# Kernel tuning notes

Measured on AMD Instinct MI355X. Metric: run time of the kernel, lower is better.

## Reference

```python
import jax, jax.numpy as jnp
import numpy as np

N_HEADS = 16
PROJ_DIM = 64  # per-head dim
DIM = N_HEADS * PROJ_DIM  # 1024


def setup_inputs() -> dict:
    key = jax.random.key(0)
    k1, k2, k3, k4, k5 = jax.random.split(key, 5)
    N, L = 2, 2048
    scale = 1.0 / np.sqrt(DIM)
    return {
        "query": jax.random.normal(k1, (N, L, DIM), dtype=jnp.float32),
        "key": jax.random.normal(k2, (N, L, DIM), dtype=jnp.float32),
        "Wq": jax.random.normal(k3, (DIM, DIM), dtype=jnp.float32) * scale,
        "Wk": jax.random.normal(k4, (DIM, DIM), dtype=jnp.float32) * scale,
        "Wv": jax.random.normal(k5, (DIM, DIM), dtype=jnp.float32) * scale,
    }


def reference(query, key, Wq, Wk, Wv):
    # Causal linear-complexity attention (mask=True branch, left_first=False).
    N, Lq, _ = query.shape
    Lk = key.shape[1]
    H, Dh = N_HEADS, PROJ_DIM
    # torch Linear: x @ W.T ; reshape to (N, H, L, Dh)
    q = (query @ Wq.T).reshape(N, Lq, H, Dh).transpose(0, 2, 1, 3)
    k = (key @ Wk.T).reshape(N, Lk, H, Dh).transpose(0, 2, 1, 3)
    v = (key @ Wv.T).reshape(N, Lk, H, Dh).transpose(0, 2, 1, 3)
    q = jax.nn.softmax(q, axis=-1)
    k = jax.nn.softmax(k, axis=-1)
    # right[t] = sum_{s<=t} k_s^T v_s  : (N,H,Lk,Dh,Dh) cumulative outer products
    S = jnp.cumsum(jnp.einsum('nhti,nhtj->nhtij', k, v), axis=2)
    out = jnp.einsum('nhti,nhtij->nhtj', q, S)  # (N,H,Lq,Dh)
    return out.transpose(0, 2, 1, 3).reshape(N, Lq, H * Dh)
```

## Files before the change

kernel.cpp:

```cpp
#include <hip/hip_runtime.h>


constexpr int DIM  = 1024;
constexpr int H    = 16;
constexpr int DH   = 64;
constexpr int LSEQ = 2048;
constexpr int NB   = 2;
constexpr int MTOK = NB * LSEQ;
constexpr int CS   = 64;
constexpr int NC   = LSEQ / CS;

typedef __bf16 bf16x8 __attribute__((ext_vector_type(8)));
typedef float floatx4 __attribute__((ext_vector_type(4)));
typedef unsigned short ushort_t;

__device__ __forceinline__ ushort_t f2bf(float f) {
  unsigned int u = __float_as_uint(f);
  u += 0x7FFFu + ((u >> 16) & 1u);
  return (ushort_t)(u >> 16);
}

__device__ __forceinline__ void async16(void* lds, const void* g) {
  __builtin_amdgcn_global_load_lds(
      (const __attribute__((address_space(1))) unsigned int*)g,
      (__attribute__((address_space(3))) unsigned int*)lds, 16, 0, 0);
}

__device__ __forceinline__ bf16x8 tfrag(const unsigned int* T, int row, int uoff) {
  union { bf16x8 v; unsigned int u[4]; } r;
  const unsigned int* p = T + row * 33 + uoff;
  r.u[0] = p[0]; r.u[1] = p[1]; r.u[2] = p[2]; r.u[3] = p[3];
  return r.v;
}

__device__ __forceinline__ void transpose_tile(const ushort_t* g, unsigned int* TT, int tid) {
  const int ic = tid & 7, tp = tid >> 3;
  const ushort_t* r0 = g + (size_t)(2 * tp) * DIM + ic * 8;
  union { uint4 q; ushort_t u[8]; } a0, a1;
  a0.q = *(const uint4*)r0;
  a1.q = *(const uint4*)(r0 + DIM);
#pragma unroll
  for (int j = 0; j < 8; j++)
    TT[(8 * ic + j) * 33 + tp] = (unsigned int)a0.u[j] | ((unsigned int)a1.u[j] << 16);
}

__global__ __launch_bounds__(256) void cast_all(const float* __restrict__ q,
                                                const float* __restrict__ k,
                                                const float* __restrict__ wq,
                                                const float* __restrict__ wk,
                                                const float* __restrict__ wv,
                                                ushort_t* __restrict__ xbf,
                                                ushort_t* __restrict__ wbf) {
  const int seg = blockIdx.y;
  const float* src;
  ushort_t* dst;
  int n4;
  if (seg == 0)      { src = q;  dst = xbf;                  n4 = (4 << 20) / 4; }
  else if (seg == 1) { src = k;  dst = xbf + (4 << 20);      n4 = (4 << 20) / 4; }
  else if (seg == 2) { src = wq; dst = wbf;                  n4 = (1 << 20) / 4; }
  else if (seg == 3) { src = wk; dst = wbf + (1 << 20);      n4 = (1 << 20) / 4; }
  else               { src = wv; dst = wbf + (2 << 20);      n4 = (1 << 20) / 4; }
  for (int i = blockIdx.x * 256 + threadIdx.x; i < n4; i += gridDim.x * 256) {
    const float4 f = ((const float4*)src)[i];
    ((ushort4*)dst)[i] = make_ushort4(f2bf(f.x), f2bf(f.y), f2bf(f.z), f2bf(f.w));
  }
}

struct Stage2 { ushort_t As[256 * 32]; ushort_t Ws[256 * 32]; };
union SMemU { Stage2 st[2]; ushort_t CsB[64 * 264]; };

__global__ __launch_bounds__(512, 2) void gemm_fused(const ushort_t* __restrict__ xbf,
                                                     const ushort_t* __restrict__ wbf,
                                                     ushort_t* __restrict__ qp,
                                                     ushort_t* __restrict__ kp,
                                                     ushort_t* __restrict__ vp) {
  __shared__ SMemU sm;
  const int tid = threadIdx.x;

  const int xcd   = blockIdx.x & 7;
  const int local = blockIdx.x >> 3;
  const int T     = xcd * 24 + local;
  const int z     = T >> 6;
  const int rem   = T & 63;
  const int bm    = (rem >> 2) * 256;
  const int bn    = (rem & 3) * 256;

  const ushort_t* A = xbf + (z ? (size_t)(4 << 20) : 0);
  const ushort_t* W = wbf + (size_t)z * (1 << 20);
  ushort_t* C = (z == 0) ? qp : ((z == 1) ? kp : vp);

  const int lane  = tid & 63;
  const int wid   = tid >> 6;
  const int wr    = wid >> 2, wc = wid & 3;
  const int row16 = lane & 15, quad = lane >> 4;

  floatx4 acc[8][4] = {};

  const int srow = tid >> 2;
  const int lc   = (tid & 3) ^ ((srow ^ (srow >> 2)) & 3);
  const ushort_t* pA0 = A + (size_t)(bm + srow) * DIM + lc * 8;
  const ushort_t* pA1 = A + (size_t)(bm + 128 + srow) * DIM + lc * 8;
  const ushort_t* pW0 = W + (size_t)(bn + srow) * DIM + lc * 8;
  const ushort_t* pW1 = W + (size_t)(bn + 128 + srow) * DIM + lc * 8;

#define STAGEB(B, kt)                                         \
  {                                                           \
    ushort_t* As_ = sm.st[B].As;                              \
    ushort_t* Ws_ = sm.st[B].Ws;                              \
    const int ko = (kt) * 32;                                 \
    async16(As_ + tid * 8,         pA0 + ko);                 \
    async16(As_ + (tid + 512) * 8, pA1 + ko);                 \
    async16(Ws_ + tid * 8,         pW0 + ko);                 \
    async16(Ws_ + (tid + 512) * 8, pW1 + ko);                 \
  }

  const int xq    = quad ^ ((row16 ^ (row16 >> 2)) & 3);
  const int aBase = (wr * 128 + row16) * 32 + xq * 8;
  const int bBase = (wc * 64 + row16) * 32 + xq * 8;

  bf16x8 aF0[8], bF0[4], aF1[8], bF1[4];

#define READB(B, AF, BF)                                                      \
  {                                                                           \
    _Pragma("unroll")                                                         \
    for (int mt = 0; mt < 8; mt++)                                            \
      AF[mt] = *(const bf16x8*)&sm.st[B].As[aBase + mt * 512];                \
    _Pragma("unroll")                                                         \
    for (int nt = 0; nt < 4; nt++)                                            \
      BF[nt] = *(const bf16x8*)&sm.st[B].Ws[bBase + nt * 512];                \
  }

#define MFMAB(AF, BF)                                                         \
  {                                                                           \
    _Pragma("unroll")                                                         \
    for (int mt = 0; mt < 8; mt++)                                            \
      _Pragma("unroll")                                                       \
      for (int nt = 0; nt < 4; nt++)                                          \
        acc[mt][nt] = __builtin_amdgcn_mfma_f32_16x16x32_bf16(                \
            AF[mt], BF[nt], acc[mt][nt], 0, 0, 0);                            \
  }

  STAGEB(0, 0);
  STAGEB(1, 1);
  asm volatile("s_waitcnt vmcnt(4)" ::: "memory");
  __builtin_amdgcn_s_barrier();
  READB(0, aF0, bF0);

#pragma unroll
  for (int kt = 0; kt < 32; ++kt) {
    asm volatile("s_waitcnt lgkmcnt(0)" ::: "memory");
    __builtin_amdgcn_s_barrier();
    if (kt + 2 < 32) {
      if ((kt & 1) == 0) { STAGEB(0, kt + 2); } else { STAGEB(1, kt + 2); }
    }
    if (kt + 1 < 32) {
      if (kt + 2 < 32) { asm volatile("s_waitcnt vmcnt(4)" ::: "memory"); }
      else             { asm volatile("s_waitcnt vmcnt(0)" ::: "memory"); }
      __builtin_amdgcn_s_barrier();
      if ((kt & 1) == 0) { READB(1, aF1, bF1); } else { READB(0, aF0, bF0); }
    }
    if ((kt & 1) == 0) { MFMAB(aF0, bF0); } else { MFMAB(aF1, bF1); }
  }
#undef STAGEB
#undef READB
#undef MFMAB

  if (z < 2) {
#pragma unroll
    for (int mt = 0; mt < 8; mt++)
#pragma unroll
      for (int r = 0; r < 4; r++) {
        float m = fmaxf(fmaxf(acc[mt][0][r], acc[mt][1][r]),
                        fmaxf(acc[mt][2][r], acc[mt][3][r]));
#pragma unroll
        for (int o = 1; o < 16; o <<= 1) m = fmaxf(m, __shfl_xor(m, o, 64));
        float e[4], s = 0.f;
#pragma unroll
        for (int nt = 0; nt < 4; nt++) { e[nt] = __expf(acc[mt][nt][r] - m); s += e[nt]; }
#pragma unroll
        for (int o = 1; o < 16; o <<= 1) s += __shfl_xor(s, o, 64);
        const float inv = 1.f / s;
#pragma unroll
        for (int nt = 0; nt < 4; nt++) acc[mt][nt][r] = e[nt] * inv;
      }
  }

#pragma unroll
  for (int p = 0; p < 4; ++p) {
    __syncthreads();
    if (wr == (p >> 1)) {
      const int mh = (p & 1) * 4;
#pragma unroll
      for (int m4 = 0; m4 < 4; m4++)
#pragma unroll
        for (int nt = 0; nt < 4; nt++)
#pragma unroll
          for (int r = 0; r < 4; r++)
            sm.CsB[(m4 * 16 + quad * 4 + r) * 264 + wc * 64 + nt * 16 + row16] =
                f2bf(acc[mh + m4][nt][r]);
    }
    __syncthreads();
#pragma unroll
    for (int it = 0; it < 4; it++) {
      const int ch = tid + it * 512;
      const int row = ch >> 5, ic = ch & 31;
      *(uint4*)&C[(size_t)(bm + p * 64 + row) * DIM + bn + ic * 8] =
          *(const uint4*)&sm.CsB[row * 264 + ic * 8];
    }
  }
}

__global__ __launch_bounds__(256) void chunk_T(const ushort_t* __restrict__ kp,
                                               const ushort_t* __restrict__ vp,
                                               float* __restrict__ cs) {
  __shared__ unsigned int KT[64 * 33];
  __shared__ unsigned int VT[64 * 33];
  const int c = blockIdx.x, h = blockIdx.y, n = blockIdx.z;
  const int tid = threadIdx.x;
  const size_t gbase = ((size_t)(n * LSEQ + c * CS)) * DIM + h * DH;

  transpose_tile(kp + gbase, KT, tid);
  transpose_tile(vp + gbase, VT, tid);
  __syncthreads();

  const int lane = tid & 63, wid = tid >> 6;
  const int row16 = lane & 15, quad = lane >> 4;

  floatx4 acc[4] = {};
#pragma unroll
  for (int ks = 0; ks < 2; ks++) {
    const bf16x8 a = tfrag(VT, wid * 16 + row16, ks * 16 + quad * 4);
#pragma unroll
    for (int nt = 0; nt < 4; nt++) {
      const bf16x8 b = tfrag(KT, nt * 16 + row16, ks * 16 + quad * 4);
      acc[nt] = __builtin_amdgcn_mfma_f32_16x16x32_bf16(a, b, acc[nt], 0, 0, 0);
    }
  }
  float* outp = cs + ((size_t)((n * H + h) * NC + c)) * (DH * DH);
#pragma unroll
  for (int nt = 0; nt < 4; nt++)
#pragma unroll
    for (int r = 0; r < 4; r++)
      outp[(wid * 16 + quad * 4 + r) * DH + nt * 16 + row16] = acc[nt][r];
}

__global__ __launch_bounds__(256) void prefix_chunks(const float* __restrict__ cs,
                                                     ushort_t* __restrict__ csb) {
  const int nh = blockIdx.x >> 4;
  const int e  = (blockIdx.x & 15) * 256 + threadIdx.x;
  const float* bf_ = cs + (size_t)nh * NC * (DH * DH) + e;
  ushort_t* bb = csb + (size_t)nh * NC * (DH * DH) + e;
  float run = 0.f;
#pragma unroll
  for (int c = 0; c < NC; c++) {
    const float cur = bf_[(size_t)c * (DH * DH)];
    bb[(size_t)c * (DH * DH)] = f2bf(run);
    run += cur;
  }
}

__global__ __launch_bounds__(256) void attn_mfma(const ushort_t* __restrict__ qp,
                                                 const ushort_t* __restrict__ kp,
                                                 const ushort_t* __restrict__ vp,
                                                 const ushort_t* __restrict__ csb,
                                                 float* __restrict__ out) {
  __shared__ ushort_t Qs[64 * 72];
  __shared__ ushort_t Ks[64 * 72];
  __shared__ ushort_t Ts[64 * 72];
  __shared__ unsigned int VT[64 * 33];
  __shared__ ushort_t Pb[64 * 72];
  const int c = blockIdx.x, h = blockIdx.y, n = blockIdx.z;
  const int tid = threadIdx.x;
  const size_t gbase = ((size_t)(n * LSEQ + c * CS)) * DIM + h * DH;
  const size_t cbase = ((size_t)((n * H + h) * NC + c)) * (DH * DH);

#pragma unroll
  for (int it = 0; it < 2; it++) {
    const int ch = tid + it * 256;
    const int row = ch >> 3, ic = ch & 7;
    *(uint4*)&Qs[row * 72 + ic * 8] = *(const uint4*)&qp[gbase + (size_t)row * DIM + ic * 8];
    *(uint4*)&Ks[row * 72 + ic * 8] = *(const uint4*)&kp[gbase + (size_t)row * DIM + ic * 8];
    *(uint4*)&Ts[row * 72 + ic * 8] = *(const uint4*)&csb[cbase + (size_t)row * DH + ic * 8];
  }
  transpose_tile(vp + gbase, VT, tid);
  __syncthreads();

  const int lane = tid & 63, wid = tid >> 6;
  const int row16 = lane & 15, quad = lane >> 4;
  const int t0 = wid * 16;

  floatx4 acc[4] = {};
  floatx4 pacc[4] = {};

#pragma unroll
  for (int ks = 0; ks < 2; ks++) {
    const bf16x8 aq = *(const bf16x8*)&Qs[(t0 + row16) * 72 + ks * 32 + quad * 8];
#pragma unroll
    for (int nt = 0; nt < 4; nt++) {
      const bf16x8 bt = *(const bf16x8*)&Ts[(nt * 16 + row16) * 72 + ks * 32 + quad * 8];
      acc[nt] = __builtin_amdgcn_mfma_f32_16x16x32_bf16(aq, bt, acc[nt], 0, 0, 0);
      const bf16x8 bk = *(const bf16x8*)&Ks[(nt * 16 + row16) * 72 + ks * 32 + quad * 8];
      pacc[nt] = __builtin_amdgcn_mfma_f32_16x16x32_bf16(aq, bk, pacc[nt], 0, 0, 0);
    }
  }
#pragma unroll
  for (int nt = 0; nt < 4; nt++)
#pragma unroll
    for (int r = 0; r < 4; r++) {
      const int t = t0 + quad * 4 + r, s = nt * 16 + row16;
      Pb[t * 72 + s] = f2bf((s <= t) ? pacc[nt][r] : 0.f);
    }
  __syncthreads();

#pragma unroll
  for (int ks = 0; ks < 2; ks++) {
    const bf16x8 ap = *(const bf16x8*)&Pb[(t0 + row16) * 72 + ks * 32 + quad * 8];
#pragma unroll
    for (int nt = 0; nt < 4; nt++) {
      const bf16x8 bv = tfrag(VT, nt * 16 + row16, ks * 16 + quad * 4);
      acc[nt] = __builtin_amdgcn_mfma_f32_16x16x32_bf16(ap, bv, acc[nt], 0, 0, 0);
    }
  }

#pragma unroll
  for (int nt = 0; nt < 4; nt++)
#pragma unroll
    for (int r = 0; r < 4; r++)
      out[gbase + (size_t)(t0 + quad * 4 + r) * DIM + nt * 16 + row16] = acc[nt][r];
}

extern "C" void kernel_launch(void* const* d_in, const int* in_sizes, int n_in,
                              void* d_out, int out_size, void* d_ws, size_t ws_size,
                              hipStream_t stream) {
  const float* query = (const float*)d_in[0];
  const float* key   = (const float*)d_in[1];
  const float* Wq    = (const float*)d_in[2];
  const float* Wk    = (const float*)d_in[3];
  const float* Wv    = (const float*)d_in[4];
  float* out = (float*)d_out;

  const size_t PM = (size_t)4 << 20;
  ushort_t* qp = (ushort_t*)d_ws;
  ushort_t* kp = qp + PM;
  ushort_t* vp = kp + PM;
  float*    cs = (float*)(vp + PM);
  ushort_t* csb = (ushort_t*)(cs + PM);
  ushort_t* xbf = (ushort_t*)cs;
  ushort_t* wbf = (ushort_t*)out;

  cast_all<<<dim3(512, 5), 256, 0, stream>>>(query, key, Wq, Wk, Wv, xbf, wbf);

  gemm_fused<<<dim3(192), 512, 0, stream>>>(xbf, wbf, qp, kp, vp);

  chunk_T<<<dim3(NC, H, NB), 256, 0, stream>>>(kp, vp, cs);
  prefix_chunks<<<dim3(NB * H * 16), 256, 0, stream>>>(cs, csb);
  attn_mfma<<<dim3(NC, H, NB), 256, 0, stream>>>(qp, kp, vp, csb, out);
}
```

Measured before the change: 156.3 us.

## Restructure projection GEMM mainloop with 64-wide K tiles and interleaved MFMA phases

Replaces the double-buffered 32-wide K loop with 64-wide K tiles in a flat 128KB shared buffer, using an 8-way XOR swizzle. Each iteration is split into four MFMA phases, separated by barriers and wrapped in s_setprio. Fragment reads and async global-to-LDS loads for the next tile are interleaved between the phases. The goal is to halve the number of loop iterations and hide load latency behind MFMA work. The larger LDS footprint likely allows only one block per CU, despite launch_bounds requesting two.

```diff
diff --git a/kernel.cpp b/kernel.cpp
--- a/kernel.cpp
+++ b/kernel.cpp
@@ -66,15 +66,12 @@
   }
 }
 
-struct Stage2 { ushort_t As[256 * 32]; ushort_t Ws[256 * 32]; };
-union SMemU { Stage2 st[2]; ushort_t CsB[64 * 264]; };
-
 __global__ __launch_bounds__(512, 2) void gemm_fused(const ushort_t* __restrict__ xbf,
                                                      const ushort_t* __restrict__ wbf,
                                                      ushort_t* __restrict__ qp,
                                                      ushort_t* __restrict__ kp,
                                                      ushort_t* __restrict__ vp) {
-  __shared__ SMemU sm;
+  __shared__ __align__(16) ushort_t sh[65536];
   const int tid = threadIdx.x;
 
   const int xcd   = blockIdx.x & 7;
@@ -96,74 +93,105 @@
 
   floatx4 acc[8][4] = {};
 
-  const int srow = tid >> 2;
-  const int lc   = (tid & 3) ^ ((srow ^ (srow >> 2)) & 3);
-  const ushort_t* pA0 = A + (size_t)(bm + srow) * DIM + lc * 8;
-  const ushort_t* pA1 = A + (size_t)(bm + 128 + srow) * DIM + lc * 8;
-  const ushort_t* pW0 = W + (size_t)(bn + srow) * DIM + lc * 8;
-  const ushort_t* pW1 = W + (size_t)(bn + 128 + srow) * DIM + lc * 8;
-
-#define STAGEB(B, kt)                                         \
-  {                                                           \
-    ushort_t* As_ = sm.st[B].As;                              \
-    ushort_t* Ws_ = sm.st[B].Ws;                              \
-    const int ko = (kt) * 32;                                 \
-    async16(As_ + tid * 8,         pA0 + ko);                 \
-    async16(As_ + (tid + 512) * 8, pA1 + ko);                 \
-    async16(Ws_ + tid * 8,         pW0 + ko);                 \
-    async16(Ws_ + (tid + 512) * 8, pW1 + ko);                 \
-  }
-
-  const int xq    = quad ^ ((row16 ^ (row16 >> 2)) & 3);
-  const int aBase = (wr * 128 + row16) * 32 + xq * 8;
-  const int bBase = (wc * 64 + row16) * 32 + xq * 8;
-
-  bf16x8 aF0[8], bF0[4], aF1[8], bF1[4];
-
-#define READB(B, AF, BF)                                                      \
+  const int srow = tid >> 3;
+  const int lc   = (tid & 7) ^ (srow & 7);
+  const ushort_t* pA[2][2];
+  const ushort_t* pB[2][2];
+#pragma unroll
+  for (int h = 0; h < 2; h++)
+#pragma unroll
+    for (int rnd = 0; rnd < 2; rnd++) {
+      pA[h][rnd] = A + (size_t)(bm + h * 128 + rnd * 64 + srow) * DIM + lc * 8;
+      pB[h][rnd] = W + (size_t)(bn + h * 128 + rnd * 64 + srow) * DIM + lc * 8;
+    }
+  char* shW = (char*)sh;
+
+#define STG(b, ism, h, kt)                                          \
+  {                                                                 \
+    char* d_ = shW + (b) * 65536 + (ism) * 32768 + (h) * 16384 + tid * 16; \
+    async16(d_,        ((ism) ? pB : pA)[h][0] + (size_t)(kt) * 64);       \
+    async16(d_ + 8192, ((ism) ? pB : pA)[h][1] + (size_t)(kt) * 64);       \
+  }
+
+  const int key = row16 & 7;
+  const int xc0 = (quad ^ key) * 16;
+  const int xc1 = ((4 + quad) ^ key) * 16;
+  const int aOff = wr * 16384 + row16 * 128;
+  const int bOff = 32768 + (wc >> 1) * 16384 + (wc & 1) * 8192 + row16 * 128;
+  const char* shR = (const char*)sh;
+
+  bf16x8 aF[4][2], bF[4][2];
+
+#define RD_A4(p, base)                                                        \
   {                                                                           \
     _Pragma("unroll")                                                         \
-    for (int mt = 0; mt < 8; mt++)                                            \
-      AF[mt] = *(const bf16x8*)&sm.st[B].As[aBase + mt * 512];                \
-    _Pragma("unroll")                                                         \
-    for (int nt = 0; nt < 4; nt++)                                            \
-      BF[nt] = *(const bf16x8*)&sm.st[B].Ws[bBase + nt * 512];                \
-  }
-
-#define MFMAB(AF, BF)                                                         \
+    for (int mt = 0; mt < 4; mt++) {                                          \
+      aF[mt][0] = *(const bf16x8*)(shR + (p) * 65536 + aOff + ((base) + mt) * 2048 + xc0); \
+      aF[mt][1] = *(const bf16x8*)(shR + (p) * 65536 + aOff + ((base) + mt) * 2048 + xc1); \
+    }                                                                         \
+  }
+#define RD_B2(p, base)                                                        \
   {                                                                           \
     _Pragma("unroll")                                                         \
-    for (int mt = 0; mt < 8; mt++)                                            \
+    for (int j = 0; j < 2; j++) {                                             \
+      bF[(base) + j][0] = *(const bf16x8*)(shR + (p) * 65536 + bOff + ((base) + j) * 2048 + xc0); \
+      bF[(base) + j][1] = *(const bf16x8*)(shR + (p) * 65536 + bOff + ((base) + j) * 2048 + xc1); \
+    }                                                                         \
+  }
+#define MFMA8(mb, nb)                                                         \
+  {                                                                           \
+    _Pragma("unroll")                                                         \
+    for (int mt = 0; mt < 4; mt++)                                            \
       _Pragma("unroll")                                                       \
-      for (int nt = 0; nt < 4; nt++)                                          \
-        acc[mt][nt] = __builtin_amdgcn_mfma_f32_16x16x32_bf16(                \
-            AF[mt], BF[nt], acc[mt][nt], 0, 0, 0);                            \
-  }
-
-  STAGEB(0, 0);
-  STAGEB(1, 1);
+      for (int nt = 0; nt < 2; nt++) {                                        \
+        acc[(mb) + mt][(nb) + nt] = __builtin_amdgcn_mfma_f32_16x16x32_bf16(  \
+            aF[mt][0], bF[(nb) + nt][0], acc[(mb) + mt][(nb) + nt], 0, 0, 0); \
+        acc[(mb) + mt][(nb) + nt] = __builtin_amdgcn_mfma_f32_16x16x32_bf16(  \
+            aF[mt][1], bF[(nb) + nt][1], acc[(mb) + mt][(nb) + nt], 0, 0, 0); \
+      }                                                                       \
+  }
+#define BARD()  asm volatile("s_barrier" ::: "memory")
+#define LGKM0() asm volatile("s_waitcnt lgkmcnt(0)" ::: "memory")
+
+  STG(0, 0, 0, 0); STG(0, 1, 0, 0);
+  STG(0, 1, 1, 0); STG(0, 0, 1, 0);
+  STG(1, 0, 0, 1); STG(1, 1, 0, 1);
   asm volatile("s_waitcnt vmcnt(4)" ::: "memory");
-  __builtin_amdgcn_s_barrier();
-  READB(0, aF0, bF0);
-
-#pragma unroll
-  for (int kt = 0; kt < 32; ++kt) {
-    asm volatile("s_waitcnt lgkmcnt(0)" ::: "memory");
-    __builtin_amdgcn_s_barrier();
-    if (kt + 2 < 32) {
-      if ((kt & 1) == 0) { STAGEB(0, kt + 2); } else { STAGEB(1, kt + 2); }
-    }
-    if (kt + 1 < 32) {
-      if (kt + 2 < 32) { asm volatile("s_waitcnt vmcnt(4)" ::: "memory"); }
-      else             { asm volatile("s_waitcnt vmcnt(0)" ::: "memory"); }
-      __builtin_amdgcn_s_barrier();
-      if ((kt & 1) == 0) { READB(1, aF1, bF1); } else { READB(0, aF0, bF0); }
-    }
-    if ((kt & 1) == 0) { MFMAB(aF0, bF0); } else { MFMAB(aF1, bF1); }
-  }
-#undef STAGEB
-#undef READB
-#undef MFMAB
+  BARD();
+
+  for (int u = 0; u < 16; ++u) {
+    const int p  = u & 1;
+    const int qb = p ^ 1;
+    RD_A4(p, 0); RD_B2(p, 0);
+    if (u + 1 < 16) { STG(qb, 1, 1, u + 1); STG(qb, 0, 1, u + 1); }
+    BARD(); LGKM0();
+    __builtin_amdgcn_s_setprio(1); MFMA8(0, 0); __builtin_amdgcn_s_setprio(0);
+    BARD();
+    RD_B2(p, 2);
+    BARD(); LGKM0();
+    __builtin_amdgcn_s_setprio(1); MFMA8(0, 2); __builtin_amdgcn_s_setprio(0);
+    BARD();
+    RD_A4(p, 4);
+    BARD(); LGKM0();
+    __builtin_amdgcn_s_setprio(1); MFMA8(4, 0); __builtin_amdgcn_s_setprio(0);
+    BARD();
+    if (u + 2 < 16) {
+      STG(p, 0, 0, u + 2); STG(p, 1, 0, u + 2);
+      asm volatile("s_waitcnt vmcnt(4)" ::: "memory");
+    } else {
+      asm volatile("s_waitcnt vmcnt(0)" ::: "memory");
+    }
+    BARD();
+    __builtin_amdgcn_s_setprio(1); MFMA8(4, 2); __builtin_amdgcn_s_setprio(0);
+    BARD();
+  }
+#undef STG
+#undef RD_A4
+#undef RD_B2
+#undef MFMA8
+#undef BARD
+#undef LGKM0
+  __syncthreads();
 
   if (z < 2) {
 #pragma unroll
@@ -185,18 +213,19 @@
       }
   }
 
-#pragma unroll
-  for (int p = 0; p < 4; ++p) {
+  ushort_t* CsB = sh;
+#pragma unroll
+  for (int p4 = 0; p4 < 4; ++p4) {
     __syncthreads();
-    if (wr == (p >> 1)) {
-      const int mh = (p & 1) * 4;
+    if (wr == (p4 >> 1)) {
+      const int mh = (p4 & 1) * 4;
 #pragma unroll
       for (int m4 = 0; m4 < 4; m4++)
 #pragma unroll
         for (int nt = 0; nt < 4; nt++)
 #pragma unroll
           for (int r = 0; r < 4; r++)
-            sm.CsB[(m4 * 16 + quad * 4 + r) * 264 + wc * 64 + nt * 16 + row16] =
+            CsB[(m4 * 16 + quad * 4 + r) * 264 + wc * 64 + nt * 16 + row16] =
                 f2bf(acc[mh + m4][nt][r]);
     }
     __syncthreads();
@@ -204,8 +233,8 @@
     for (int it = 0; it < 4; it++) {
       const int ch = tid + it * 512;
       const int row = ch >> 5, ic = ch & 31;
-      *(uint4*)&C[(size_t)(bm + p * 64 + row) * DIM + bn + ic * 8] =
-          *(const uint4*)&sm.CsB[row * 264 + ic * 8];
+      *(uint4*)&C[(size_t)(bm + p4 * 64 + row) * DIM + bn + ic * 8] =
+          *(const uint4*)&CsB[row * 264 + ic * 8];
     }
   }
 }
```

Measured after the change: 158.5 us. About the same (+1.4%).
